# Performance work log

Measured on AMD Instinct MI355X. Metric: run time of the kernel, lower is better.

Reference implementation:

```python
import jax, jax.numpy as jnp
import numpy as np

GRID_SPACING = 0.5  # tf.constant(0.5)


def _mlp(x, W1, b1, W2, b2, W3, b3):
    # tiny base_model: 3 -> H -> H -> 1, positive output (softplus head)
    h = jnp.tanh(x @ W1 + b1)
    h = jnp.tanh(h @ W2 + b2)
    return jax.nn.softplus(h @ W3 + b3)


def setup_inputs() -> dict:
    key = jax.random.key(0)
    ks = jax.random.split(key, 8)
    nx = ny = nz = 128
    N = nx * ny * nz
    Ns = (nx - 1) * (ny - 1) * (nz - 1)
    B, H = 32768, 128
    DATAX = jax.random.uniform(ks[0], (N, 3), dtype=jnp.float32)
    DATAF = jax.random.uniform(ks[1], (N, 1), dtype=jnp.float32)
    STAGX = jax.random.uniform(ks[2], (Ns, 3), dtype=jnp.float32)
    LAPLF = jax.random.uniform(ks[3], (nx - 2, ny - 2, nz - 2), dtype=jnp.float32)
    center_indices = jax.random.randint(ks[4], (B,), 0, N, dtype=jnp.int32)
    W1 = jax.random.normal(ks[5], (3, H), dtype=jnp.float32) * 0.5
    W2 = jax.random.normal(ks[6], (H, H), dtype=jnp.float32) * (1.0 / np.sqrt(H))
    W3 = jax.random.normal(ks[7], (H, 1), dtype=jnp.float32) * (1.0 / np.sqrt(H))
    return {
        'DATAX': DATAX, 'DATAF': DATAF, 'STAGX': STAGX, 'LAPLF': LAPLF,
        'loss_m_weight': jnp.full((1,), 0.5, dtype=jnp.float32),
        'W1': W1, 'b1': jnp.zeros((H,), jnp.float32),
        'W2': W2, 'b2': jnp.zeros((H,), jnp.float32),
        'W3': W3, 'b3': jnp.zeros((1,), jnp.float32),
        'center_indices': center_indices,
    }


def reference(DATAX, DATAF, STAGX, LAPLF, loss_m_weight,
              W1, b1, W2, b2, W3, b3, center_indices):
    nxm2, nym2, nzm2 = LAPLF.shape
    nx, ny, nz = nxm2 + 2, nym2 + 2, nzm2 + 2
    N = nx * ny * nz
    Ns = (nx - 1) * (ny - 1) * (nz - 1)
    ci = center_indices.astype(jnp.int32)

    # decode flat id (z-major: z*nx*ny + y*nx + x)
    i_z = ci // (nx * ny)
    rem = ci % (nx * ny)
    i_y = rem // nx
    i_x = rem % nx
    valid = ((i_x >= 1) & (i_x < nx - 1) & (i_y >= 1) & (i_y < ny - 1)
             & (i_z >= 1) & (i_z < nz - 1))

    # 8 original-grid corners: dx,dy,dz in {-1,1}, dz fastest (list-comp order)
    off = jnp.array([-1, 1], jnp.int32)
    dd = jnp.stack(jnp.meshgrid(off, off, off, indexing='ij'), -1).reshape(8, 3)
    ox = i_x[:, None] + dd[None, :, 0]
    oy = i_y[:, None] + dd[None, :, 1]
    oz = i_z[:, None] + dd[None, :, 2]
    flat_o = jnp.clip(oz * nx * ny + oy * nx + ox, 0, N - 1)  # [B,8]

    # 8 staggered-grid corners: dx,dy,dz in {-1,0}, flat = x*ny'*nz' + y*nz' + z
    offs = jnp.array([-1, 0], jnp.int32)
    ds = jnp.stack(jnp.meshgrid(offs, offs, offs, indexing='ij'), -1).reshape(8, 3)
    sx = i_x[:, None] + ds[None, :, 0]
    sy = i_y[:, None] + ds[None, :, 1]
    sz = i_z[:, None] + ds[None, :, 2]
    flat_s = jnp.clip(sx * (ny - 1) * (nz - 1) + sy * (nz - 1) + sz, 0, Ns - 1)

    fo = _mlp(DATAX[flat_o], W1, b1, W2, b2, W3, b3)[..., 0]  # [B,8]
    fs = _mlp(STAGX[flat_s], W1, b1, W2, b2, W3, b3)[..., 0]  # [B,8]

    # diagonals of the [2,2,2] cube: (000,111),(010,101),(001,110),(011,100)
    ia = jnp.array([0, 2, 1, 3])
    ib = jnp.array([7, 5, 6, 4])
    num = jnp.abs(fo[:, ia] + fo[:, ib] - fs[:, ia] - fs[:, ib])
    den = fo[:, ia] + fo[:, ib] + fs[:, ia] + fs[:, ib]
    delta = 3.0 * (GRID_SPACING ** 2)
    lap = jnp.sum(num / den, axis=1) / (3.0 * delta)  # [B]

    flat_l = jnp.clip((i_x - 1) * nym2 * nzm2 + (i_y - 1) * nzm2 + (i_z - 1),
                      0, nxm2 * nym2 * nzm2 - 1)
    dlap = LAPLF.reshape(-1)[flat_l] - lap
    m = valid.astype(dlap.dtype)
    loss_m = loss_m_weight[0] * (jnp.sum(jnp.square(dlap) * m)
                                 / jnp.maximum(jnp.sum(m), 1.0))

    pred = _mlp(DATAX[ci], W1, b1, W2, b2, W3, b3)[:, 0]
    loss_e = jnp.mean(jnp.abs(pred - DATAF[ci][:, 0]))
    return loss_e + loss_m
```

## Files before the change

### kernel.cpp

```cpp
#include <hip/hip_runtime.h>

#define NXC   128
#define NXY   16384
#define NTOT  2097152
#define NS    2048383
#define SXY   16129
#define SYC   127
#define LXY   15876
#define LTOT  2000376

typedef __bf16 bf16x8 __attribute__((ext_vector_type(8)));
typedef float f32x4 __attribute__((ext_vector_type(4)));

__device__ __forceinline__ float fast_rcp(float x) {
#if __has_builtin(__builtin_amdgcn_rcpf)
  return __builtin_amdgcn_rcpf(x);
#else
  return 1.0f / x;
#endif
}

__device__ __forceinline__ float fast_tanh(float x) {
  float e = __expf(2.0f * x);
  return 1.0f - 2.0f * fast_rcp(e + 1.0f);
}

__device__ __forceinline__ float softplus_f(float x) {
  float a = fabsf(x);
  return fmaxf(x, 0.0f) + __logf(1.0f + __expf(-a));
}

__device__ __forceinline__ void ld8(const float* p, float* o) {
  float4 a = *reinterpret_cast<const float4*>(p);
  float4 b = *reinterpret_cast<const float4*>(p + 4);
  o[0] = a.x; o[1] = a.y; o[2] = a.z; o[3] = a.w;
  o[4] = b.x; o[5] = b.y; o[6] = b.z; o[7] = b.w;
}

__global__ __launch_bounds__(256, 2) void mlp_kernel(
    const float* __restrict__ DATAX, const float* __restrict__ STAGX,
    const int* __restrict__ CI,
    const float* __restrict__ W1, const float* __restrict__ B1,
    const float* __restrict__ W2, const float* __restrict__ B2,
    const float* __restrict__ W3, const float* __restrict__ B3,
    float* __restrict__ fout)
{
  __shared__ __align__(16) __bf16 w2t[16384];
  __shared__ __align__(16) float w1s[384];
  __shared__ __align__(16) float b1s[128];
  __shared__ float b2s[128];
  __shared__ float w3s[128];

  const int tid  = threadIdx.x;
  const int lane = tid & 63;
  const int wid  = tid >> 6;
  const int cl   = lane & 15;
  const int g    = lane >> 4;

  const int group = (blockIdx.x << 2) + wid;
  const int gbase = group << 6;
  const int p = gbase + lane;
  const unsigned bb = (unsigned)p / 17u;
  const int t = p - (int)bb * 17;
  const int ci = CI[bb];

  for (int idx4 = tid; idx4 < 4096; idx4 += 256) {
    const int idx = idx4 << 2;
    float4 w = *reinterpret_cast<const float4*>(&W2[idx]);
    const int k = idx >> 7, j0 = idx & 127;
    const int c = k >> 3, e = k & 7;
    const float wv[4] = {w.x, w.y, w.z, w.w};
    #pragma unroll
    for (int q = 0; q < 4; ++q) {
      const int j = j0 + q;
      w2t[(j << 7) + (((c ^ (j & 15)) << 3) | e)] = (__bf16)wv[q];
    }
  }
  for (int idx = tid; idx < 384; idx += 256) w1s[idx] = W1[idx];
  if (tid < 128) { b1s[tid] = B1[tid]; b2s[tid] = B2[tid]; w3s[tid] = W3[tid]; }

  const int iz = ci >> 14, rem = ci & 16383, iy = rem >> 7, ix = rem & 127;
  const float* xp;
  if (t < 8) {
    int ox = ix + ((t & 4) ? 1 : -1);
    int oy = iy + ((t & 2) ? 1 : -1);
    int oz = iz + ((t & 1) ? 1 : -1);
    int fl = oz * NXY + oy * NXC + ox;
    fl = min(max(fl, 0), NTOT - 1);
    xp = DATAX + 3 * fl;
  } else if (t < 16) {
    int ts = t - 8;
    int sx = ix + ((ts & 4) ? 0 : -1);
    int sy = iy + ((ts & 2) ? 0 : -1);
    int sz = iz + ((ts & 1) ? 0 : -1);
    int fl = sx * SXY + sy * SYC + sz;
    fl = min(max(fl, 0), NS - 1);
    xp = STAGX + 3 * fl;
  } else {
    xp = DATAX + 3 * ci;
  }
  const float px = xp[0], py = xp[1], pz = xp[2];

  __syncthreads();

  float b2r[8], w3r[8];
  #pragma unroll
  for (int nt = 0; nt < 8; ++nt) {
    b2r[nt] = b2s[cl + (nt << 4)];
    w3r[nt] = w3s[cl + (nt << 4)];
  }
  const float b3v = B3[0];

  float rxv[4], ryv[4], rzv[4];
  #pragma unroll
  for (int mt = 0; mt < 4; ++mt) {
    int src = (mt << 4) + cl;
    rxv[mt] = __shfl(px, src);
    ryv[mt] = __shfl(py, src);
    rzv[mt] = __shfl(pz, src);
  }

  bf16x8 A[4][4];
  #pragma unroll
  for (int kt = 0; kt < 4; ++kt) {
    int k0 = (kt << 5) + (g << 3);
    float wx[8], wy[8], wz[8], bv[8];
    ld8(&w1s[k0], wx);
    ld8(&w1s[128 + k0], wy);
    ld8(&w1s[256 + k0], wz);
    ld8(&b1s[k0], bv);
    #pragma unroll
    for (int mt = 0; mt < 4; ++mt) {
      #pragma unroll
      for (int e = 0; e < 8; ++e) {
        float pre = fmaf(rxv[mt], wx[e],
                    fmaf(ryv[mt], wy[e],
                    fmaf(rzv[mt], wz[e], bv[e])));
        A[mt][kt][e] = (__bf16)fast_tanh(pre);
      }
    }
  }

  float s[4][4];
  #pragma unroll
  for (int mt = 0; mt < 4; ++mt)
    #pragma unroll
    for (int r = 0; r < 4; ++r) s[mt][r] = 0.f;

  #pragma unroll
  for (int nt = 0; nt < 8; ++nt) {
    f32x4 cc[4];
    #pragma unroll
    for (int mt = 0; mt < 4; ++mt) {
      f32x4 z = {0.f, 0.f, 0.f, 0.f};
      cc[mt] = z;
    }
    const int row = (nt << 4) + cl;
    #pragma unroll
    for (int kt = 0; kt < 4; ++kt) {
      int chunk = (kt << 2) + g;
      bf16x8 bfv = *reinterpret_cast<const bf16x8*>(
          &w2t[(row << 7) + ((chunk ^ cl) << 3)]);
      #pragma unroll
      for (int mt = 0; mt < 4; ++mt)
        cc[mt] = __builtin_amdgcn_mfma_f32_16x16x32_bf16(A[mt][kt], bfv, cc[mt], 0, 0, 0);
    }
    #pragma unroll
    for (int mt = 0; mt < 4; ++mt) {
      #pragma unroll
      for (int r = 0; r < 4; ++r) {
        float h2 = fast_tanh(cc[mt][r] + b2r[nt]);
        s[mt][r] = fmaf(h2, w3r[nt], s[mt][r]);
      }
    }
  }

  #pragma unroll
  for (int mt = 0; mt < 4; ++mt) {
    #pragma unroll
    for (int r = 0; r < 4; ++r) {
      float v = s[mt][r];
      v += __shfl_xor(v, 1);
      v += __shfl_xor(v, 2);
      v += __shfl_xor(v, 4);
      v += __shfl_xor(v, 8);
      s[mt][r] = v;
    }
  }
  if (cl == 0) {
    #pragma unroll
    for (int mt = 0; mt < 4; ++mt) {
      int base = gbase + (mt << 4) + (g << 2);
      float4 o;
      o.x = softplus_f(s[mt][0] + b3v);
      o.y = softplus_f(s[mt][1] + b3v);
      o.z = softplus_f(s[mt][2] + b3v);
      o.w = softplus_f(s[mt][3] + b3v);
      *reinterpret_cast<float4*>(&fout[base]) = o;
    }
  }
}

__global__ __launch_bounds__(256) void reduce1(
    const float* __restrict__ f, const int* __restrict__ CI,
    const float* __restrict__ LAPLF, const float* __restrict__ DATAF,
    float* __restrict__ partials, int B)
{
  const int tid = threadIdx.x;
  const int b = blockIdx.x * 256 + tid;
  float sq = 0.f, mv = 0.f, ae = 0.f;
  if (b < B) {
    int ci = CI[b];
    int iz = ci >> 14, rem = ci & 16383, iy = rem >> 7, ix = rem & 127;
    bool valid = (ix >= 1) & (ix < 127) & (iy >= 1) & (iy < 127) &
                 (iz >= 1) & (iz < 127);
    const float* fb = f + b * 17;
    float fo[8], fs[8];
    #pragma unroll
    for (int i = 0; i < 8; ++i) { fo[i] = fb[i]; fs[i] = fb[8 + i]; }
    float pred = fb[16];
    const int ia[4] = {0, 2, 1, 3};
    const int ib[4] = {7, 5, 6, 4};
    float lap = 0.f;
    #pragma unroll
    for (int r = 0; r < 4; ++r) {
      float aa = fo[ia[r]] + fo[ib[r]];
      float bs = fs[ia[r]] + fs[ib[r]];
      lap += fabsf(aa - bs) / (aa + bs);
    }
    lap *= (1.0f / 2.25f);
    int fl = (ix - 1) * LXY + (iy - 1) * 126 + (iz - 1);
    fl = min(max(fl, 0), LTOT - 1);
    float dlap = LAPLF[fl] - lap;
    if (valid) { sq = dlap * dlap; mv = 1.f; }
    ae = fabsf(pred - DATAF[ci]);
  }
  #pragma unroll
  for (int msk = 32; msk >= 1; msk >>= 1) {
    sq += __shfl_xor(sq, msk);
    mv += __shfl_xor(mv, msk);
    ae += __shfl_xor(ae, msk);
  }
  __shared__ float rs[3][4];
  int lane = tid & 63, wd = tid >> 6;
  if (lane == 0) { rs[0][wd] = sq; rs[1][wd] = mv; rs[2][wd] = ae; }
  __syncthreads();
  if (tid == 0) {
    partials[blockIdx.x * 3 + 0] = rs[0][0] + rs[0][1] + rs[0][2] + rs[0][3];
    partials[blockIdx.x * 3 + 1] = rs[1][0] + rs[1][1] + rs[1][2] + rs[1][3];
    partials[blockIdx.x * 3 + 2] = rs[2][0] + rs[2][1] + rs[2][2] + rs[2][3];
  }
}

__global__ __launch_bounds__(128) void reduce2(
    const float* __restrict__ partials, const float* __restrict__ lw,
    float* __restrict__ out, int np, float invB)
{
  const int t = threadIdx.x;
  float sq = 0.f, mv = 0.f, ae = 0.f;
  for (int i = t; i < np; i += 128) {
    sq += partials[3 * i + 0];
    mv += partials[3 * i + 1];
    ae += partials[3 * i + 2];
  }
  #pragma unroll
  for (int msk = 32; msk >= 1; msk >>= 1) {
    sq += __shfl_xor(sq, msk);
    mv += __shfl_xor(mv, msk);
    ae += __shfl_xor(ae, msk);
  }
  __shared__ float rs[3][2];
  int lane = t & 63, wd = t >> 6;
  if (lane == 0) { rs[0][wd] = sq; rs[1][wd] = mv; rs[2][wd] = ae; }
  __syncthreads();
  if (t == 0) {
    float S = rs[0][0] + rs[0][1];
    float M = rs[1][0] + rs[1][1];
    float A = rs[2][0] + rs[2][1];
    out[0] = lw[0] * (S / fmaxf(M, 1.0f)) + A * invB;
  }
}

extern "C" void kernel_launch(void* const* d_in, const int* in_sizes, int n_in,
                              void* d_out, int out_size, void* d_ws, size_t ws_size,
                              hipStream_t stream) {
  const float* DATAX = (const float*)d_in[0];
  const float* DATAF = (const float*)d_in[1];
  const float* STAGX = (const float*)d_in[2];
  const float* LAPLF = (const float*)d_in[3];
  const float* LW    = (const float*)d_in[4];
  const float* W1    = (const float*)d_in[5];
  const float* B1    = (const float*)d_in[6];
  const float* W2    = (const float*)d_in[7];
  const float* B2    = (const float*)d_in[8];
  const float* W3    = (const float*)d_in[9];
  const float* B3    = (const float*)d_in[10];
  const int*   CI    = (const int*)d_in[11];

  const int B = in_sizes[11];
  const int P = 17 * B;
  const int ngroups = P >> 6;
  const int nblocks = ngroups >> 2;

  float* fbuf = (float*)d_ws;
  float* partials = fbuf + P;

  mlp_kernel<<<nblocks, 256, 0, stream>>>(DATAX, STAGX, CI, W1, B1, W2, B2,
                                          W3, B3, fbuf);
  const int nb2 = (B + 255) >> 8;
  reduce1<<<nb2, 256, 0, stream>>>(fbuf, CI, LAPLF, DATAF, partials, B);
  reduce2<<<1, 128, 0, stream>>>(partials, LW, (float*)d_out, nb2, 1.0f / (float)B);
}
```

Before: 77.55 us.

## Precompute bf16 swizzled W2 once and stream weights into LDS via global_load_lds

Adds a small pre-kernel that converts W2 to bf16 in the swizzled layout the MFMA loop reads and packs W1/b1/b2/w3 into one contiguous buffer. Each MLP block then copies these straight into shared memory with direct global-to-LDS loads instead of converting and scattering fp32 weights per block. It also folds the b2 bias into the MFMA accumulator seed and uses inline v_rcp_f32 for the tanh. The cost is an extra kernel launch and reliance on the LDS layout of global_load_lds lining up with the swizzle.

```diff
diff --git a/kernel.cpp b/kernel.cpp
--- a/kernel.cpp
+++ b/kernel.cpp
@@ -1,4 +1,5 @@
 #include <hip/hip_runtime.h>
+#include <stdint.h>
 
 #define NXC   128
 #define NXY   16384
@@ -12,17 +13,18 @@
 typedef __bf16 bf16x8 __attribute__((ext_vector_type(8)));
 typedef float f32x4 __attribute__((ext_vector_type(4)));
 
-__device__ __forceinline__ float fast_rcp(float x) {
-#if __has_builtin(__builtin_amdgcn_rcpf)
-  return __builtin_amdgcn_rcpf(x);
-#else
-  return 1.0f / x;
-#endif
+typedef const __attribute__((address_space(1))) uint32_t* gas_t;
+typedef __attribute__((address_space(3))) uint32_t* las_t;
+
+__device__ __forceinline__ float rcp_hw(float x) {
+  float r;
+  asm("v_rcp_f32 %0, %1" : "=v"(r) : "v"(x));
+  return r;
 }
 
 __device__ __forceinline__ float fast_tanh(float x) {
   float e = __expf(2.0f * x);
-  return 1.0f - 2.0f * fast_rcp(e + 1.0f);
+  return 1.0f - 2.0f * rcp_hw(e + 1.0f);
 }
 
 __device__ __forceinline__ float softplus_f(float x) {
@@ -37,19 +39,40 @@
   o[4] = b.x; o[5] = b.y; o[6] = b.z; o[7] = b.w;
 }
 
+__global__ __launch_bounds__(256) void conv_kernel(
+    const float* __restrict__ W1, const float* __restrict__ B1,
+    const float* __restrict__ W2, const float* __restrict__ B2,
+    const float* __restrict__ W3,
+    __bf16* __restrict__ w2pre, float* __restrict__ smallpre)
+{
+  const int n = blockIdx.x * 256 + threadIdx.x;
+  if (n < 2048) {
+    const int c = n >> 7, j = n & 127;
+    bf16x8 v;
+    #pragma unroll
+    for (int e = 0; e < 8; ++e) v[e] = (__bf16)W2[(8 * c + e) * 128 + j];
+    *reinterpret_cast<bf16x8*>(&w2pre[(j << 7) + (((c ^ (j & 15)) & 15) << 3)]) = v;
+  }
+  if (blockIdx.x == 0) {
+    for (int i = threadIdx.x; i < 768; i += 256) {
+      float v;
+      if (i < 384)      v = W1[i];
+      else if (i < 512) v = B1[i - 384];
+      else if (i < 640) v = B2[i - 512];
+      else              v = W3[i - 640];
+      smallpre[i] = v;
+    }
+  }
+}
+
 __global__ __launch_bounds__(256, 2) void mlp_kernel(
     const float* __restrict__ DATAX, const float* __restrict__ STAGX,
     const int* __restrict__ CI,
-    const float* __restrict__ W1, const float* __restrict__ B1,
-    const float* __restrict__ W2, const float* __restrict__ B2,
-    const float* __restrict__ W3, const float* __restrict__ B3,
-    float* __restrict__ fout)
+    const __bf16* __restrict__ w2pre, const float* __restrict__ smallpre,
+    const float* __restrict__ B3, float* __restrict__ fout)
 {
   __shared__ __align__(16) __bf16 w2t[16384];
-  __shared__ __align__(16) float w1s[384];
-  __shared__ __align__(16) float b1s[128];
-  __shared__ float b2s[128];
-  __shared__ float w3s[128];
+  __shared__ __align__(16) float smallb[768];
 
   const int tid  = threadIdx.x;
   const int lane = tid & 63;
@@ -64,20 +87,26 @@
   const int t = p - (int)bb * 17;
   const int ci = CI[bb];
 
-  for (int idx4 = tid; idx4 < 4096; idx4 += 256) {
-    const int idx = idx4 << 2;
-    float4 w = *reinterpret_cast<const float4*>(&W2[idx]);
-    const int k = idx >> 7, j0 = idx & 127;
-    const int c = k >> 3, e = k & 7;
-    const float wv[4] = {w.x, w.y, w.z, w.w};
-    #pragma unroll
-    for (int q = 0; q < 4; ++q) {
-      const int j = j0 + q;
-      w2t[(j << 7) + (((c ^ (j & 15)) << 3) | e)] = (__bf16)wv[q];
-    }
-  }
-  for (int idx = tid; idx < 384; idx += 256) w1s[idx] = W1[idx];
-  if (tid < 128) { b1s[tid] = B1[tid]; b2s[tid] = B2[tid]; w3s[tid] = W3[tid]; }
+  {
+    const char* gsrc = (const char*)w2pre + (wid << 13) + (lane << 4);
+    char*       ldst = (char*)w2t + (wid << 13);
+    #pragma unroll
+    for (int i = 0; i < 8; ++i) {
+      __builtin_amdgcn_global_load_lds(
+          (gas_t)(const void*)(gsrc + (i << 10)),
+          (las_t)(void*)(ldst + (i << 10)), 16, 0, 0);
+    }
+    if (wid == 3) {
+      const char* gs = (const char*)smallpre + (lane << 4);
+      char*       ld = (char*)smallb;
+      #pragma unroll
+      for (int i = 0; i < 3; ++i) {
+        __builtin_amdgcn_global_load_lds(
+            (gas_t)(const void*)(gs + (i << 10)),
+            (las_t)(void*)(ld + (i << 10)), 16, 0, 0);
+      }
+    }
+  }
 
   const int iz = ci >> 14, rem = ci & 16383, iy = rem >> 7, ix = rem & 127;
   const float* xp;
@@ -100,8 +129,14 @@
     xp = DATAX + 3 * ci;
   }
   const float px = xp[0], py = xp[1], pz = xp[2];
+  const float b3v = B3[0];
 
   __syncthreads();
+
+  const float* w1s = smallb;
+  const float* b1s = smallb + 384;
+  const float* b2s = smallb + 512;
+  const float* w3s = smallb + 640;
 
   float b2r[8], w3r[8];
   #pragma unroll
@@ -109,7 +144,6 @@
     b2r[nt] = b2s[cl + (nt << 4)];
     w3r[nt] = w3s[cl + (nt << 4)];
   }
-  const float b3v = B3[0];
 
   float rxv[4], ryv[4], rzv[4];
   #pragma unroll
@@ -152,8 +186,8 @@
     f32x4 cc[4];
     #pragma unroll
     for (int mt = 0; mt < 4; ++mt) {
-      f32x4 z = {0.f, 0.f, 0.f, 0.f};
-      cc[mt] = z;
+      f32x4 seed = {b2r[nt], b2r[nt], b2r[nt], b2r[nt]};
+      cc[mt] = seed;
     }
     const int row = (nt << 4) + cl;
     #pragma unroll
@@ -169,7 +203,7 @@
     for (int mt = 0; mt < 4; ++mt) {
       #pragma unroll
       for (int r = 0; r < 4; ++r) {
-        float h2 = fast_tanh(cc[mt][r] + b2r[nt]);
+        float h2 = fast_tanh(cc[mt][r]);
         s[mt][r] = fmaf(h2, w3r[nt], s[mt][r]);
       }
     }
@@ -302,11 +336,14 @@
   const int ngroups = P >> 6;
   const int nblocks = ngroups >> 2;
 
-  float* fbuf = (float*)d_ws;
-  float* partials = fbuf + P;
-
-  mlp_kernel<<<nblocks, 256, 0, stream>>>(DATAX, STAGX, CI, W1, B1, W2, B2,
-                                          W3, B3, fbuf);
+  __bf16* w2pre    = (__bf16*)d_ws;
+  float*  smallpre = (float*)((char*)d_ws + 32768);
+  float*  fbuf     = (float*)((char*)d_ws + 36864);
+  float*  partials = fbuf + P;
+
+  conv_kernel<<<8, 256, 0, stream>>>(W1, B1, W2, B2, W3, w2pre, smallpre);
+  mlp_kernel<<<nblocks, 256, 0, stream>>>(DATAX, STAGX, CI, w2pre, smallpre,
+                                          B3, fbuf);
   const int nb2 = (B + 255) >> 8;
   reduce1<<<nb2, 256, 0, stream>>>(fbuf, CI, LAPLF, DATAF, partials, B);
   reduce2<<<1, 128, 0, stream>>>(partials, LW, (float*)d_out, nb2, 1.0f / (float)B);
```

Measured after the change: 68.95 us. 11.1% less time.
